# Kernel optimization log

Measured on AMD Instinct MI355X. Metric: run time of the kernel, lower is better.

The kernel has to match this reference:

```python
import jax, jax.numpy as jnp
from jax import lax
import numpy as np

TAU = 10.0      # tauSr == tauRef
THR = 1.0       # theta
WIDTH = 1.0     # tauRho (surrogate width)
SCALE = 1.0     # scaleRho (surrogate scale)
DECAY = float(np.exp(-1.0 / TAU))


@jax.custom_vjp
def _heaviside(v):
    # spike = 1[v >= theta]
    return (v >= THR).astype(v.dtype)

def _heaviside_fwd(v):
    return _heaviside(v), v

def _heaviside_bwd(v, g):
    # SLAYER exponential surrogate pdf: scaleRho/tauRho * exp(-|v-theta|/tauRho)
    return (g * (SCALE / WIDTH) * jnp.exp(-jnp.abs(v - THR) / WIDTH),)

_heaviside.defvjp(_heaviside_fwd, _heaviside_bwd)


def _conv2d(x, w, pad):
    # x: (B, Cin, H, W), w: (Cout, Cin, kh, kw); SLAYER convs have no bias
    return lax.conv_general_dilated(
        x, w, window_strides=(1, 1), padding=[(pad, pad), (pad, pad)],
        dimension_numbers=("NCHW", "OIHW", "NCHW"))


def _sumpool(x, k):
    # SLAYER pool = sum over kxk window (times a learned scalar applied outside)
    B, C, H, W = x.shape
    return x.reshape(B, C, H // k, k, W // k, k).sum(axis=(3, 5))


def _psp(seq):
    # exponential synaptic (PSP) filter along time: s[t] = a*s[t-1] + x[t]
    a = jnp.asarray(DECAY, seq.dtype)
    def step(s, x_t):
        s = a * s + x_t
        return s, s
    _, out = lax.scan(step, jnp.zeros_like(seq[0]), seq)
    return out  # (T, ...)


def _spikes(u):
    # thresholded spiking with decaying refractory feedback (scaleRef=1):
    # v[t] = u[t] - r[t]; s[t] = 1[v >= theta]; r[t+1] = b*(r[t] + theta*s[t])
    b = jnp.asarray(DECAY, u.dtype)
    def step(r, u_t):
        s = _heaviside(u_t - r)
        r_next = b * (r + THR * s)
        return r_next, s
    _, out = lax.scan(step, jnp.zeros_like(u[0]), u)
    return out  # (T, ...)


def _forward(x, conv1_w, conv2_w, lin_w, w_pool1, w_pool2):
    N, T, C, H, W = x.shape  # (64, 100, 2, 32, 32)
    h = _conv2d(x.reshape(N * T, C, H, W), conv1_w, 2)        # (NT, 4, 32, 32)
    h = _sumpool(h, 4) * w_pool1                               # (NT, 4, 8, 8)
    h = h.reshape(N, T, 4, 8, 8).swapaxes(0, 1)                # (T, N, 4, 8, 8)
    s1 = _spikes(_psp(h))                                      # (T, N, 4, 8, 8)
    h2 = _conv2d(s1.reshape(T * N, 4, 8, 8), conv2_w, 1)       # (TN, 8, 8, 8)
    h2 = (_sumpool(h2, 2) * w_pool2).reshape(T, N, 8, 4, 4)    # (T, N, 8, 4, 4)
    s2 = _spikes(_psp(h2))                                     # (T, N, 8, 4, 4)
    # dense = full-spatial conv (2, 8, 4, 4) -> (N, T, 2)
    return jnp.einsum("tnchw,ochw->nto", s2, lin_w)


def setup_inputs() -> dict:
    key = jax.random.key(0)
    ks = jax.random.split(key, 4)
    x = (jax.random.uniform(ks[0], (64, 100, 2, 32, 32)) < 0.1).astype(jnp.float32)
    conv1_w = jax.random.normal(ks[1], (4, 2, 5, 5), jnp.float32) * 0.3
    conv2_w = jax.random.normal(ks[2], (8, 4, 3, 3), jnp.float32) * 0.3
    lin_w = jax.random.normal(ks[3], (2, 8, 4, 4), jnp.float32) * 0.3
    w_pool1 = jnp.float32(1.0 / 16.0)  # 1.1*theta / (16 * 1.1)
    w_pool2 = jnp.float32(1.0 / 4.0)   # 1.1*theta / (4 * 1.1)
    return {"x": x, "conv1_w": conv1_w, "conv2_w": conv2_w, "lin_w": lin_w,
            "w_pool1": w_pool1, "w_pool2": w_pool2}


def reference(x, conv1_w, conv2_w, lin_w, w_pool1, w_pool2):
    return _forward(x, conv1_w, conv2_w, lin_w, w_pool1, w_pool2)
```

## Files before the change

### kernel.cpp

```cpp
#include <hip/hip_runtime.h>


#define DECAY 0.9048374180359595f

#define BAR_LGKM() asm volatile("s_waitcnt lgkmcnt(0)\n\ts_barrier" ::: "memory")
#define FENCE_LGKM() asm volatile("s_waitcnt lgkmcnt(0)" ::: "memory")

__global__ __launch_bounds__(128) void k0_fold(const float* __restrict__ w1,
        const float* __restrict__ w2, const float* __restrict__ wp1,
        const float* __restrict__ wp2, float* __restrict__ wl1,
        float* __restrict__ wl2) {
    const int tid = threadIdx.x;
    const float p1 = wp1[0], p2 = wp2[0];
    for (int idx = tid; idx < 512; idx += 128) {
        const int f = idx & 7, c = (idx >> 3) & 3, e = (idx >> 5) & 7, cin = idx >> 8;
        const int cc = c * 2 + cin;
        int alo = e - 3; if (alo < 0) alo = 0;
        int ahi = e;     if (ahi > 4) ahi = 4;
        int blo = f - 3; if (blo < 0) blo = 0;
        int bhi = f;     if (bhi > 4) bhi = 4;
        float s = 0.f;
        for (int a = alo; a <= ahi; ++a)
            for (int b = blo; b <= bhi; ++b)
                s += w1[cc * 25 + a * 5 + b];
        wl1[(cin * 8 + e) * 32 + c * 8 + f] = s * p1;
    }
    for (int idx = tid; idx < 512; idx += 128) {
        const int c2 = idx & 7, f = (idx >> 3) & 3, e = (idx >> 5) & 3, cin = idx >> 7;
        int alo = e - 1; if (alo < 0) alo = 0;
        int ahi = e;     if (ahi > 2) ahi = 2;
        int blo = f - 1; if (blo < 0) blo = 0;
        int bhi = f;     if (bhi > 2) bhi = 2;
        float s = 0.f;
        for (int aa = alo; aa <= ahi; ++aa)
            for (int bb = blo; bb <= bhi; ++bb)
                s += w2[((c2 * 4 + cin) * 3 + aa) * 3 + bb];
        wl2[c2 * 68 + cin * 16 + e * 4 + f] = s * p2;
    }
}

__global__ __launch_bounds__(64) void k1(const float* __restrict__ x,
        const float* __restrict__ wg, float* __restrict__ u1) {
    __shared__ __align__(16) float xs[2 * 1296];
    __shared__ __align__(16) float wl[512];
    const int lane = threadIdx.x;
    const int frame = blockIdx.x;
    const int n = frame / 100, t = frame % 100;

    *(float4*)(wl + 4 * lane)       = *(const float4*)(wg + 4 * lane);
    *(float4*)(wl + 256 + 4 * lane) = *(const float4*)(wg + 256 + 4 * lane);

    #pragma unroll
    for (int m0 = 0; m0 < 128; m0 += 64) {
        const int m = m0 + lane;
        if (m < 72) {
            const int cin = m / 36, rem = m % 36;
            const int rr = rem / 9, q4 = rem % 9;
            const int pr = (rr == 0) ? 0 : (rr == 1) ? 9 : (rr == 2) ? 26 : 35;
            *(float4*)(xs + cin * 1296 + pr * 36 + q4 * 4) = make_float4(0.f, 0.f, 0.f, 0.f);
        }
    }
    #pragma unroll
    for (int m0 = 0; m0 < 192; m0 += 64) {
        const int m = m0 + lane;
        if (m < 144) {
            const int cin = m / 72, rem = m % 72;
            const int side = rem & 1, pr = rem >> 1;
            *(float2*)(xs + cin * 1296 + pr * 36 + side * 34) = make_float2(0.f, 0.f);
        }
    }
    const float4* xg = (const float4*)(x + (size_t)frame * 2048);
    #pragma unroll
    for (int q = 0; q < 8; ++q) {
        const int m = q * 64 + lane;
        const float4 v = xg[m];
        const int li = 4 * m;
        const int cin = li >> 10, row = (li >> 5) & 31, col = li & 31;
        const int r = row + 2;
        const int pr = (r & 3) * 9 + (r >> 2);
        float* d = xs + cin * 1296 + pr * 36 + col + 2;
        *(float2*)(d)     = make_float2(v.x, v.y);
        *(float2*)(d + 2) = make_float2(v.z, v.w);
    }
    FENCE_LGKM();

    const int cp = lane >> 5;
    const int i  = (lane >> 2) & 7;
    const int jh = (lane >> 1) & 1;
    const int eh = lane & 1;

    float acc[2][4] = {{0.f, 0.f, 0.f, 0.f}, {0.f, 0.f, 0.f, 0.f}};
    const float* tb = xs + (i + eh) * 36 + jh * 16;
    #pragma unroll
    for (int cin = 0; cin < 2; ++cin) {
        #pragma unroll
        for (int et = 0; et < 4; ++et) {
            const int ro = cin * 1296 + et * 9 * 36;
            float xr[20];
            #pragma unroll
            for (int b = 0; b < 5; ++b)
                *(float4*)(xr + 4 * b) = *(const float4*)(tb + ro + 4 * b);
            float wv[16];
            const float* wp = wl + (cin * 8 + eh * 4 + et) * 32 + cp * 16;
            #pragma unroll
            for (int q = 0; q < 4; ++q)
                *(float4*)(wv + 4 * q) = *(const float4*)(wp + 4 * q);
            #pragma unroll
            for (int cl = 0; cl < 2; ++cl) {
                #pragma unroll
                for (int jj = 0; jj < 4; ++jj) {
                    const int o = 4 * jj;
                    acc[cl][jj] += xr[o]*wv[cl*8]     + xr[o+1]*wv[cl*8+1]
                                 + xr[o+2]*wv[cl*8+2] + xr[o+3]*wv[cl*8+3]
                                 + xr[o+4]*wv[cl*8+4] + xr[o+5]*wv[cl*8+5]
                                 + xr[o+6]*wv[cl*8+6] + xr[o+7]*wv[cl*8+7];
                }
            }
        }
    }
    #pragma unroll
    for (int cl = 0; cl < 2; ++cl)
        #pragma unroll
        for (int jj = 0; jj < 4; ++jj)
            acc[cl][jj] += __shfl_xor(acc[cl][jj], 1);

    const float o0 = eh ? acc[1][0] : acc[0][0];
    const float o1 = eh ? acc[1][1] : acc[0][1];
    const float o2 = eh ? acc[1][2] : acc[0][2];
    const float o3 = eh ? acc[1][3] : acc[0][3];
    *(float4*)(u1 + (size_t)t * 16384 + n * 256 + (2 * cp + eh) * 64 + i * 8 + jh * 4) =
        make_float4(o0, o1, o2, o3);
}

__global__ __launch_bounds__(256) void kf(const float* __restrict__ u1,
        const float* __restrict__ wl2g, const float* __restrict__ lw,
        float* __restrict__ out) {
    __shared__ __align__(16) float ls1[8 * 660];
    __shared__ __align__(16) float ls2[8 * 132];
    __shared__ __align__(16) float wl[544];
    const int tid = threadIdx.x, n = blockIdx.x;
    const int wave = tid >> 6, l64 = tid & 63;
    const int sub = tid >> 5, l = tid & 31;
    const float a = DECAY;

    if (tid < 136) *(float4*)(wl + 4 * tid) = *(const float4*)(wl2g + 4 * tid);
    for (int m = tid; m < 1320; m += 256)
        *(float4*)(ls1 + 4 * m) = make_float4(0.f, 0.f, 0.f, 0.f);

    const int cs = tid >> 6, rowi = (tid >> 3) & 7, col = tid & 7;
    const int pr1 = (((rowi + 1) & 1) * 5) + ((rowi + 1) >> 1);
    const int woff = cs * 160 + pr1 * 16 + 4 + col;
    const float* up = u1 + n * 256 + tid;

    const int c2 = l >> 2, i2 = l & 3;
    const float* wb = wl + c2 * 68;

    const float dw0 = lw[l64], dw1 = lw[64 + l64], dw2 = lw[128 + l64], dw3 = lw[192 + l64];

    float psp = 0.f, rr = 0.f;
    float psp2 = 0.f, rr2 = 0.f;

    float vbuf[8];
    #pragma unroll
    for (int k = 0; k < 8; ++k) vbuf[k] = up[(size_t)k * 16384];

    BAR_LGKM();

    #pragma unroll 1
    for (int rd = 0; rd < 13; ++rd) {
        const int t0 = rd * 8;
        const int cnt = (rd == 12) ? 4 : 8;

        float sreg[8];
        #pragma unroll
        for (int k = 0; k < 8; ++k) {
            if (k < cnt) {
                psp = a * psp + vbuf[k];
                const float vv = psp - rr;
                const float s = (vv >= 1.f) ? 1.f : 0.f;
                rr = a * (rr + s);
                sreg[k] = s;
            }
        }
        #pragma unroll
        for (int k = 0; k < 8; ++k) {
            const int tt = t0 + 8 + k;
            if (tt < 100) vbuf[k] = up[(size_t)tt * 16384];
        }
        #pragma unroll
        for (int k = 0; k < 8; ++k)
            if (k < cnt) ls1[k * 660 + woff] = sreg[k];
        BAR_LGKM();

        if (sub < cnt) {
            const float* tb = ls1 + sub * 660 + i2 * 16;
            float acc[4] = {0.f, 0.f, 0.f, 0.f};
            #pragma unroll
            for (int cin = 0; cin < 4; ++cin) {
                #pragma unroll
                for (int e = 0; e < 4; ++e) {
                    const int C = cin * 160 + ((e & 1) * 5 + (e >> 1)) * 16;
                    float xr[16];
                    #pragma unroll
                    for (int b = 0; b < 4; ++b)
                        *(float4*)(xr + 4 * b) = *(const float4*)(tb + C + 4 * b);
                    float wv[4];
                    *(float4*)(wv) = *(const float4*)(wb + cin * 16 + e * 4);
                    #pragma unroll
                    for (int j = 0; j < 4; ++j) {
                        #pragma unroll
                        for (int f = 0; f < 4; ++f)
                            acc[j] += xr[2 * j + f + 3] * wv[f];
                    }
                }
            }
            *(float4*)(ls2 + sub * 132 + c2 * 16 + i2 * 4) =
                make_float4(acc[0], acc[1], acc[2], acc[3]);
        }
        BAR_LGKM();

        if (tid < 128) {
            #pragma unroll
            for (int k = 0; k < 8; ++k) {
                if (k < cnt) {
                    const float u = ls2[k * 132 + tid];
                    psp2 = a * psp2 + u;
                    const float vv = psp2 - rr2;
                    const float s = (vv >= 1.f) ? 1.f : 0.f;
                    rr2 = a * (rr2 + s);
                    ls2[k * 132 + tid] = s;
                }
            }
        }
        BAR_LGKM();

        #pragma unroll
        for (int h = 0; h < 2; ++h) {
            const int ss = wave + 4 * h;
            if (ss < cnt) {
                const float sa = ls2[ss * 132 + l64];
                const float sb = ls2[ss * 132 + 64 + l64];
                float a0 = sa * dw0 + sb * dw1;
                float a1 = sa * dw2 + sb * dw3;
                #pragma unroll
                for (int off = 32; off > 0; off >>= 1) {
                    a0 += __shfl_down(a0, off);
                    a1 += __shfl_down(a1, off);
                }
                if (l64 == 0) {
                    const int tt = t0 + ss;
                    out[n * 200 + tt * 2]     = a0;
                    out[n * 200 + tt * 2 + 1] = a1;
                }
            }
        }
    }
}

extern "C" void kernel_launch(void* const* d_in, const int* in_sizes, int n_in,
                              void* d_out, int out_size, void* d_ws, size_t ws_size,
                              hipStream_t stream) {
    const float* x   = (const float*)d_in[0];
    const float* w1  = (const float*)d_in[1];
    const float* w2  = (const float*)d_in[2];
    const float* lw  = (const float*)d_in[3];
    const float* wp1 = (const float*)d_in[4];
    const float* wp2 = (const float*)d_in[5];

    float* u1  = (float*)d_ws;
    float* wl1 = u1 + 1638400;
    float* wl2 = wl1 + 512;
    float* out = (float*)d_out;

    k0_fold<<<1, 128, 0, stream>>>(w1, w2, wp1, wp2, wl1, wl2);
    k1<<<6400, 64, 0, stream>>>(x, wl1, u1);
    kf<<<64, 256, 0, stream>>>(u1, wl2, lw, out);
}
```

Before: 143.4 us.

## Split final spiking kernel across two blocks per sample by output channel

The fused second-layer kernel now runs two blocks per sample, each computing half of the conv2 output channels and the second spiking layer for those channels. The partial dense outputs are combined with atomicAdd, and the output is zeroed first inside the weight-fold kernel, which now launches 100 blocks. The conv2 weights are held in registers instead of shared memory, and the unused padding taps are trimmed (woff shift, 12-float loads). The aim is to double parallelism in the serial time loop, which previously ran only 64 blocks on a GPU with many more CUs. In exchange it adds atomics, duplicates the first-layer spiking work in both blocks, and leaves half the threads idle during the conv stage.

```diff
diff --git a/kernel.cpp b/kernel.cpp
--- a/kernel.cpp
+++ b/kernel.cpp
@@ -9,8 +9,10 @@
 __global__ __launch_bounds__(128) void k0_fold(const float* __restrict__ w1,
         const float* __restrict__ w2, const float* __restrict__ wp1,
         const float* __restrict__ wp2, float* __restrict__ wl1,
-        float* __restrict__ wl2) {
+        float* __restrict__ wl2, float* __restrict__ out) {
     const int tid = threadIdx.x;
+    out[blockIdx.x * 128 + tid] = 0.f;
+    if (blockIdx.x != 0) return;
     const float p1 = wp1[0], p2 = wp2[0];
     for (int idx = tid; idx < 512; idx += 128) {
         const int f = idx & 7, c = (idx >> 3) & 3, e = (idx >> 5) & 7, cin = idx >> 8;
@@ -136,26 +138,34 @@
         const float* __restrict__ wl2g, const float* __restrict__ lw,
         float* __restrict__ out) {
     __shared__ __align__(16) float ls1[8 * 660];
-    __shared__ __align__(16) float ls2[8 * 132];
-    __shared__ __align__(16) float wl[544];
-    const int tid = threadIdx.x, n = blockIdx.x;
+    __shared__ __align__(16) float ls2[8 * 68];
+    const int tid = threadIdx.x;
+    const int n = blockIdx.x >> 1, h = blockIdx.x & 1;
     const int wave = tid >> 6, l64 = tid & 63;
-    const int sub = tid >> 5, l = tid & 31;
     const float a = DECAY;
 
-    if (tid < 136) *(float4*)(wl + 4 * tid) = *(const float4*)(wl2g + 4 * tid);
     for (int m = tid; m < 1320; m += 256)
         *(float4*)(ls1 + 4 * m) = make_float4(0.f, 0.f, 0.f, 0.f);
 
     const int cs = tid >> 6, rowi = (tid >> 3) & 7, col = tid & 7;
     const int pr1 = (((rowi + 1) & 1) * 5) + ((rowi + 1) >> 1);
-    const int woff = cs * 160 + pr1 * 16 + 4 + col;
+    const int woff = cs * 160 + pr1 * 16 + 1 + col;
     const float* up = u1 + n * 256 + tid;
 
-    const int c2 = l >> 2, i2 = l & 3;
-    const float* wb = wl + c2 * 68;
-
-    const float dw0 = lw[l64], dw1 = lw[64 + l64], dw2 = lw[128 + l64], dw3 = lw[192 + l64];
+    const int sub = tid >> 4, l16 = tid & 15;
+    const int c2l = l16 >> 2, i2 = l16 & 3;
+    const int c2g = h * 4 + c2l;
+
+    float4 wreg[16];
+    {
+        const float* wbase = wl2g + c2g * 68;
+        #pragma unroll
+        for (int q = 0; q < 16; ++q)
+            wreg[q] = *(const float4*)(wbase + (q >> 2) * 16 + (q & 3) * 4);
+    }
+
+    const float dw0 = lw[h * 64 + l64];
+    const float dw1 = lw[128 + h * 64 + l64];
 
     float psp = 0.f, rr = 0.f;
     float psp2 = 0.f, rr2 = 0.f;
@@ -192,7 +202,7 @@
             if (k < cnt) ls1[k * 660 + woff] = sreg[k];
         BAR_LGKM();
 
-        if (sub < cnt) {
+        if (tid < 128 && sub < cnt) {
             const float* tb = ls1 + sub * 660 + i2 * 16;
             float acc[4] = {0.f, 0.f, 0.f, 0.f};
             #pragma unroll
@@ -200,48 +210,47 @@
                 #pragma unroll
                 for (int e = 0; e < 4; ++e) {
                     const int C = cin * 160 + ((e & 1) * 5 + (e >> 1)) * 16;
-                    float xr[16];
+                    float xr[12];
                     #pragma unroll
-                    for (int b = 0; b < 4; ++b)
+                    for (int b = 0; b < 3; ++b)
                         *(float4*)(xr + 4 * b) = *(const float4*)(tb + C + 4 * b);
-                    float wv[4];
-                    *(float4*)(wv) = *(const float4*)(wb + cin * 16 + e * 4);
+                    const float4 wf = wreg[cin * 4 + e];
                     #pragma unroll
                     for (int j = 0; j < 4; ++j) {
-                        #pragma unroll
-                        for (int f = 0; f < 4; ++f)
-                            acc[j] += xr[2 * j + f + 3] * wv[f];
+                        acc[j] += xr[2 * j]     * wf.x;
+                        acc[j] += xr[2 * j + 1] * wf.y;
+                        acc[j] += xr[2 * j + 2] * wf.z;
+                        acc[j] += xr[2 * j + 3] * wf.w;
                     }
                 }
             }
-            *(float4*)(ls2 + sub * 132 + c2 * 16 + i2 * 4) =
+            *(float4*)(ls2 + sub * 68 + c2l * 16 + i2 * 4) =
                 make_float4(acc[0], acc[1], acc[2], acc[3]);
         }
         BAR_LGKM();
 
-        if (tid < 128) {
+        if (tid < 64) {
             #pragma unroll
             for (int k = 0; k < 8; ++k) {
                 if (k < cnt) {
-                    const float u = ls2[k * 132 + tid];
+                    const float u = ls2[k * 68 + tid];
                     psp2 = a * psp2 + u;
                     const float vv = psp2 - rr2;
                     const float s = (vv >= 1.f) ? 1.f : 0.f;
                     rr2 = a * (rr2 + s);
-                    ls2[k * 132 + tid] = s;
+                    ls2[k * 68 + tid] = s;
                 }
             }
         }
         BAR_LGKM();
 
         #pragma unroll
-        for (int h = 0; h < 2; ++h) {
-            const int ss = wave + 4 * h;
+        for (int hh = 0; hh < 2; ++hh) {
+            const int ss = wave + 4 * hh;
             if (ss < cnt) {
-                const float sa = ls2[ss * 132 + l64];
-                const float sb = ls2[ss * 132 + 64 + l64];
-                float a0 = sa * dw0 + sb * dw1;
-                float a1 = sa * dw2 + sb * dw3;
+                const float sa = ls2[ss * 68 + l64];
+                float a0 = sa * dw0;
+                float a1 = sa * dw1;
                 #pragma unroll
                 for (int off = 32; off > 0; off >>= 1) {
                     a0 += __shfl_down(a0, off);
@@ -249,8 +258,8 @@
                 }
                 if (l64 == 0) {
                     const int tt = t0 + ss;
-                    out[n * 200 + tt * 2]     = a0;
-                    out[n * 200 + tt * 2 + 1] = a1;
+                    atomicAdd(&out[n * 200 + tt * 2],     a0);
+                    atomicAdd(&out[n * 200 + tt * 2 + 1], a1);
                 }
             }
         }
@@ -272,7 +281,7 @@
     float* wl2 = wl1 + 512;
     float* out = (float*)d_out;
 
-    k0_fold<<<1, 128, 0, stream>>>(w1, w2, wp1, wp2, wl1, wl2);
+    k0_fold<<<100, 128, 0, stream>>>(w1, w2, wp1, wp2, wl1, wl2, out);
     k1<<<6400, 64, 0, stream>>>(x, wl1, u1);
-    kf<<<64, 256, 0, stream>>>(u1, wl2, lw, out);
-}
+    kf<<<128, 256, 0, stream>>>(u1, wl2, lw, out);
+}
```

After: 140.7 us. Within noise of the previous version (-1.8%).
